# Performance work log

Hardware: AMD Instinct MI355X
Metric: run time of the kernel (lower is better)

Reference implementation:

```python
import jax, jax.numpy as jnp
import numpy as np

D_CUT = 5.0   # cosine-cutoff distance
SIZE = 128    # rbf size == hidden_channels (nn_dist size = in_channels)
L = 2         # num_layers
EPS = 0.0     # GIN eps (non-trainable, initial 0)


def _rbf(d):
    # d: (E,) distances -> (E, SIZE) expnorm RBF with cosine cutoff
    d = d[:, None]
    start = float(np.exp(-D_CUT))
    means = jnp.linspace(start, 1.0, SIZE)
    beta = (2.0 / SIZE * (1.0 - start)) ** (-2)
    dc = jnp.minimum(d, D_CUT)
    cutoff = 0.5 * (jnp.cos(dc * jnp.pi / D_CUT) + 1.0)
    return cutoff * jnp.exp(-beta * (jnp.exp(-d) - means) ** 2)


def setup_inputs() -> dict:
    key = jax.random.key(0)
    ks = jax.random.split(key, 40)
    it = iter(range(40))
    def k():
        return ks[next(it)]
    N, H, ED, AS = 100000, 128, 4, 4
    def w(shape, s):
        return jax.random.normal(k(), shape, jnp.float32) * s
    inp = {}
    inp['x_lig'] = jax.random.normal(k(), (N, H), jnp.float32)
    inp['x_pock'] = jax.random.normal(k(), (N, H), jnp.float32)
    for name, E in (('bond', 200000), ('lp', 400000), ('pl', 400000)):
        inp['ei_' + name] = jax.random.randint(k(), (2, E), 0, N, jnp.int32)
        inp['ew_' + name] = jax.random.uniform(k(), (E,), jnp.float32) * D_CUT
        inp['ea_' + name] = jax.random.normal(k(), (E, AS), jnp.float32)
    inp['W0'] = w((3, AS, ED), 0.5)                 # initial per-edge-type lins (no bias)
    inp['Wd'] = w((L, 3, H, 2 * H), H ** -0.5)      # RBFDistanceScaleShift lin
    inp['bd'] = jnp.zeros((L, 3, 2 * H), jnp.float32)
    inp['We'] = w((L, 3, ED, H), 0.5)               # EGINConv.lin (edge_dim -> hidden)
    inp['be'] = jnp.zeros((L, 3, H), jnp.float32)
    inp['W1'] = w((L, 3, H, H), H ** -0.5)          # nn_node MLP layer 1
    inp['b1'] = jnp.zeros((L, 3, H), jnp.float32)
    inp['W2'] = w((L, 3, H, H), H ** -0.5)          # nn_node MLP layer 2
    inp['b2'] = jnp.zeros((L, 3, H), jnp.float32)
    return inp


def reference(x_lig, x_pock, ei_bond, ew_bond, ea_bond, ei_lp, ew_lp, ea_lp,
              ei_pl, ew_pl, ea_pl, W0, Wd, bd, We, be, W1, b1, W2, b2):
    # HeteroEGIN.forward: initial per-edge-type linear on raw edge attrs (bias-free)
    ea0 = ea_bond @ W0[0]
    ea1 = ea_lp @ W0[1]
    ea2 = ea_pl @ W0[2]

    def conv(x_src, x_dst, ei, ew, ea, t, l):
        # EGINConv per edge type t, layer l
        ss = _rbf(ew) @ Wd[l, t] + bd[l, t]            # (E, 2H) scale/shift from distance
        scale, shift = jnp.split(ss, 2, axis=1)
        xj = x_src[ei[0]] + (ea @ We[l, t] + be[l, t])  # gather + edge-attr lin
        msg = jax.nn.relu(xj * scale + shift)           # gated message
        agg = jax.ops.segment_sum(msg, ei[1], num_segments=x_dst.shape[0])
        o = agg + (1.0 + EPS) * x_dst
        return jax.nn.relu(o @ W1[l, t] + b1[l, t]) @ W2[l, t] + b2[l, t]

    for l in range(L):
        # to_hetero: sum conv outputs across edge types per destination node type
        new_lig = (conv(x_lig, x_lig, ei_bond, ew_bond, ea0, 0, l)
                   + conv(x_pock, x_lig, ei_pl, ew_pl, ea2, 2, l))
        new_pock = conv(x_lig, x_pock, ei_lp, ew_lp, ea1, 1, l)
        if l < L - 1:  # BasicGNN: act between layers, none after last (jk=None)
            new_lig = jax.nn.relu(new_lig)
            new_pock = jax.nn.relu(new_pock)
        x_lig, x_pock = new_lig, new_pock
    return jnp.concatenate([x_lig, x_pock], axis=0)
```

## Files before the change

kernel.cpp:

```cpp
#include <hip/hip_runtime.h>
#include <hip/hip_bf16.h>
#include <hip/hip_fp16.h>
#include <cmath>

typedef __attribute__((ext_vector_type(8))) short short8_t;
typedef __attribute__((ext_vector_type(4))) float f32x4;

static __device__ __forceinline__ short f2bs(float f) {
    union { __hip_bfloat16 h; short s; } u;
    u.h = __float2bfloat16(f);
    return u.s;
}
static __device__ __forceinline__ float bs2f(unsigned int us) {
    union { float f; unsigned int i; } u;
    u.i = us << 16;
    return u.f;
}
static __device__ __forceinline__ unsigned int pack2bf(float a, float b) {
    return (unsigned int)(unsigned short)f2bs(a) |
           ((unsigned int)(unsigned short)f2bs(b) << 16);
}
static __device__ __forceinline__ void lds_barrier() {
    asm volatile("s_waitcnt lgkmcnt(0)\n\ts_barrier" ::: "memory");
}

__global__ void pack_kernel(const float* __restrict__ Wd,
                            const float* __restrict__ W1,
                            const float* __restrict__ W2,
                            const float* __restrict__ W0,
                            const float* __restrict__ We,
                            short* __restrict__ pWd,
                            short* __restrict__ pW1,
                            short* __restrict__ pW2,
                            float* __restrict__ Mb)
{
    const int tid = blockIdx.x * blockDim.x + threadIdx.x;
    const int stride = gridDim.x * blockDim.x;
    for (int i = tid; i < 6 * 32768; i += stride) {
        int c = i >> 15, rem = i & 32767;
        int f = rem >> 9, l = (rem >> 3) & 63, j = rem & 7;
        int kk = f >> 4, nt = f & 15;
        int k = kk * 32 + (l >> 4) * 8 + j;
        int n = nt * 16 + (l & 15);
        pWd[i] = f2bs(Wd[(size_t)c * 32768 + k * 256 + n]);
    }
    for (int i = tid; i < 6 * 16384; i += stride) {
        int c = i >> 14, rem = i & 16383;
        int f = rem >> 9, l = (rem >> 3) & 63, j = rem & 7;
        int kk = f >> 3, nt = f & 7;
        int k = kk * 32 + (l >> 4) * 8 + j;
        int n = nt * 16 + (l & 15);
        pW1[i] = f2bs(W1[(size_t)c * 16384 + k * 128 + n]);
        pW2[i] = f2bs(W2[(size_t)c * 16384 + k * 128 + n]);
    }
    for (int i = tid; i < 6 * 512; i += stride) {
        int c = i >> 9, rem = i & 511;
        int a = rem >> 7, h = rem & 127;
        int t = c % 3;
        float m = 0.f;
        #pragma unroll
        for (int j = 0; j < 4; ++j)
            m = fmaf(W0[t * 16 + a * 4 + j], We[(size_t)c * 512 + j * 128 + h], m);
        Mb[i] = m;
    }
}

__global__ void tobf16_kernel(const float* __restrict__ a, const float* __restrict__ b,
                              unsigned short* __restrict__ oa, unsigned short* __restrict__ ob,
                              int n4)
{
    int i = blockIdx.x * blockDim.x + threadIdx.x;
    const int stride = gridDim.x * blockDim.x;
    for (; i < n4; i += stride) {
        float4 va = ((const float4*)a)[i];
        uint2 pa; pa.x = pack2bf(va.x, va.y); pa.y = pack2bf(va.z, va.w);
        ((uint2*)oa)[i] = pa;
        float4 vb = ((const float4*)b)[i];
        uint2 pb; pb.x = pack2bf(vb.x, vb.y); pb.y = pack2bf(vb.z, vb.w);
        ((uint2*)ob)[i] = pb;
    }
}

__global__ void hist_kernel(const int* __restrict__ ei, int* __restrict__ cnt, int E)
{
    for (int e = blockIdx.x * blockDim.x + threadIdx.x; e < E;
         e += gridDim.x * blockDim.x)
        atomicAdd(&cnt[ei[E + e]], 1);
}

__global__ void scan1k_kernel(int* __restrict__ data, int* __restrict__ bsum, int n)
{
    __shared__ int buf[1024];
    const int gid = blockIdx.x * 1024 + threadIdx.x;
    int v = (gid < n) ? data[gid] : 0;
    buf[threadIdx.x] = v;
    __syncthreads();
    for (int off = 1; off < 1024; off <<= 1) {
        int t = (threadIdx.x >= off) ? buf[threadIdx.x - off] : 0;
        __syncthreads();
        buf[threadIdx.x] += t;
        __syncthreads();
    }
    if (gid < n) data[gid] = buf[threadIdx.x] - v;
    if (bsum && threadIdx.x == 1023) bsum[blockIdx.x] = buf[1023];
}

__global__ void scan_add_kernel(int* __restrict__ data, const int* __restrict__ bsum,
                                int* __restrict__ cursor, int n)
{
    const int gid = blockIdx.x * 1024 + threadIdx.x;
    if (gid < n) {
        int v = data[gid] + bsum[blockIdx.x];
        data[gid] = v;
        cursor[gid] = v;
    }
}

__global__ void scatter_kernel(const int* __restrict__ ei, const float* __restrict__ ew,
                               const float4* __restrict__ ea, int* __restrict__ cursor,
                               float* __restrict__ ewp, float4* __restrict__ eap,
                               int* __restrict__ srcp, int* __restrict__ dstp, int E)
{
    for (int e = blockIdx.x * blockDim.x + threadIdx.x; e < E;
         e += gridDim.x * blockDim.x) {
        int d = ei[E + e];
        int p = atomicAdd(&cursor[d], 1);
        ewp[p]  = ew[e];
        eap[p]  = ea[e];
        srcp[p] = ei[e];
        dstp[p] = d;
    }
}

__global__ __launch_bounds__(512, 2)
void edge_mfma_kernel(
    const unsigned short* __restrict__ xsb,
    const int* __restrict__ srcp, const int* __restrict__ dstp,
    const float* __restrict__ ewp, const float4* __restrict__ eap,
    const short* __restrict__ pWd, const float* __restrict__ bd,
    const float* __restrict__ Mb, const float* __restrict__ be,
    __half2* __restrict__ agg, int E, int ntiles,
    float rs, float rstep, float rbeta)
{
    __shared__ short sRbf[64 * 128];
    __shared__ __half sSS[64 * 256];

    const int t = threadIdx.x;
    const int lane = t & 63;
    const int w = t >> 6;
    const int l15 = lane & 15;
    const int l4 = lane >> 4;

    short8_t bfrag[4][2];
    #pragma unroll
    for (int kk = 0; kk < 4; ++kk)
        #pragma unroll
        for (int i = 0; i < 2; ++i)
            bfrag[kk][i] = *(const short8_t*)&pWd[((kk * 16 + 2 * w + i) * 64 + lane) * 8];
    float bdv[2];
    #pragma unroll
    for (int i = 0; i < 2; ++i) bdv[i] = bd[(2 * w + i) * 16 + l15];
    const float be0 = be[2 * lane], be1 = be[2 * lane + 1];
    float ma0[4], ma1[4];
    #pragma unroll
    for (int a = 0; a < 4; ++a) {
        ma0[a] = Mb[a * 128 + 2 * lane];
        ma1[a] = Mb[a * 128 + 2 * lane + 1];
    }

    const int stride = gridDim.x;
    int tile = blockIdx.x;
    if (tile >= ntiles) return;

    float dd_c; int dst_c; float4 ea_c;
    unsigned int gx[8];
    {
        const int e0 = tile << 6;
        int eL = e0 + lane;
        int eLc = eL < E ? eL : E - 1;
        dd_c = ewp[eLc];
        int es = e0 + w * 8 + (lane & 7);
        int esv = es < E ? es : E - 1;
        dst_c = (es < E) ? dstp[esv] : -1;
        int src_c = srcp[esv];
        ea_c = eap[esv];
        #pragma unroll
        for (int r = 0; r < 8; ++r) {
            int srn = __shfl(src_c, r);
            gx[r] = *(const unsigned int*)&xsb[(size_t)srn * 128 + lane * 2];
        }
    }

    for (; tile < ntiles; tile += stride) {
        const float edv = __expf(-dd_c);
        const float dcc = fminf(dd_c, 5.0f);
        const float cutv = 0.5f * (__cosf(dcc * 0.62831853071795864769f) + 1.0f);
        {
            char* base = (char*)sRbf + lane * 256;
            #pragma unroll
            for (int c = 0; c < 2; ++c) {
                short8_t v;
                #pragma unroll
                for (int j = 0; j < 8; ++j) {
                    float mean = rs + (float)(w * 16 + c * 8 + j) * rstep;
                    float diff = edv - mean;
                    v[j] = f2bs(cutv * __expf(-rbeta * diff * diff));
                }
                *(short8_t*)(base + ((w * 32 + c * 16) ^ ((lane & 7) << 4))) = v;
            }
        }
        unsigned int xjr[8];
        #pragma unroll
        for (int r = 0; r < 8; ++r) {
            float ea0 = __shfl(ea_c.x, r), ea1 = __shfl(ea_c.y, r);
            float ea2 = __shfl(ea_c.z, r), ea3 = __shfl(ea_c.w, r);
            unsigned int g = gx[r];
            float x0 = bs2f(g & 0xffffu), x1 = bs2f(g >> 16);
            float o0 = x0 + be0 + ea0 * ma0[0] + ea1 * ma0[1] + ea2 * ma0[2] + ea3 * ma0[3];
            float o1 = x1 + be1 + ea0 * ma1[0] + ea1 * ma1[1] + ea2 * ma1[2] + ea3 * ma1[3];
            xjr[r] = pack2bf(o0, o1);
        }

        lds_barrier();

        const int ntile = tile + stride;
        const bool has_next = ntile < ntiles;
        float dd_n = 0.f; int dst_n = -1; int src_n = 0;
        float4 ea_n = {0.f, 0.f, 0.f, 0.f};
        if (has_next) {
            const int e0n = ntile << 6;
            int eL = e0n + lane;
            int eLc = eL < E ? eL : E - 1;
            dd_n = ewp[eLc];
            int es = e0n + w * 8 + (lane & 7);
            int esv = es < E ? es : E - 1;
            dst_n = (es < E) ? dstp[esv] : -1;
            src_n = srcp[esv];
            ea_n = eap[esv];
        }
        __builtin_amdgcn_sched_barrier(0);

        f32x4 acc[4][2];
        #pragma unroll
        for (int m = 0; m < 4; ++m) {
            acc[m][0] = (f32x4){0.f, 0.f, 0.f, 0.f};
            acc[m][1] = (f32x4){0.f, 0.f, 0.f, 0.f};
        }
        #pragma unroll
        for (int kk = 0; kk < 4; ++kk) {
            short8_t af[4];
            #pragma unroll
            for (int m = 0; m < 4; ++m) {
                int row = m * 16 + l15;
                int byte = row * 256 + ((kk * 64 + l4 * 16) ^ ((row & 7) << 4));
                af[m] = *(const short8_t*)((const char*)sRbf + byte);
            }
            #pragma unroll
            for (int m = 0; m < 4; ++m)
                #pragma unroll
                for (int i = 0; i < 2; ++i)
                    acc[m][i] = __builtin_amdgcn_mfma_f32_16x16x32_bf16(
                        af[m], bfrag[kk][i], acc[m][i], 0, 0, 0);
        }

        #pragma unroll
        for (int m = 0; m < 4; ++m)
            #pragma unroll
            for (int i = 0; i < 2; ++i) {
                int col = (2 * w + i) * 16 + l15;
                #pragma unroll
                for (int r = 0; r < 4; ++r) {
                    int row = m * 16 + l4 * 4 + r;
                    int byte = row * 512 + ((col * 2) ^ ((row & 7) << 4));
                    *(__half*)((char*)sSS + byte) = __float2half(acc[m][i][r] + bdv[i]);
                }
            }

        if (has_next) {
            #pragma unroll
            for (int r = 0; r < 8; ++r) {
                int srn = __shfl(src_n, r);
                gx[r] = *(const unsigned int*)&xsb[(size_t)srn * 128 + lane * 2];
            }
        }
        const int dst_f = dst_c;
        dd_c = dd_n; dst_c = dst_n; ea_c = ea_n;

        lds_barrier();

        {
            float a0 = 0.f, a1 = 0.f;
            int rdst = __shfl(dst_f, 0);
            #pragma unroll
            for (int r = 0; r < 8; ++r) {
                int e = 8 * w + r;
                unsigned int sc = *(const unsigned int*)
                    ((const char*)sSS + e * 512 + ((lane * 4) ^ ((e & 7) << 4)));
                unsigned int sh = *(const unsigned int*)
                    ((const char*)sSS + e * 512 + ((256 + lane * 4) ^ ((e & 7) << 4)));
                float2 scf = __half22float2(*(const __half2*)&sc);
                float2 shf = __half22float2(*(const __half2*)&sh);
                unsigned int g = xjr[r];
                float x0 = bs2f(g & 0xffffu), x1 = bs2f(g >> 16);
                float m0 = fmaxf(fmaf(x0, scf.x, shf.x), 0.0f);
                float m1 = fmaxf(fmaf(x1, scf.y, shf.y), 0.0f);
                int d = __shfl(dst_f, r);
                if (d != rdst) {
                    if (rdst >= 0) {
                        __half2 hv = __floats2half2_rn(a0, a1);
                        unsigned int hb;
                        __builtin_memcpy(&hb, &hv, 4);
                        if (hb)
                            unsafeAtomicAdd(agg + (size_t)rdst * 64 + lane, hv);
                    }
                    a0 = 0.f; a1 = 0.f; rdst = d;
                }
                a0 += m0; a1 += m1;
            }
            if (rdst >= 0) {
                __half2 hv = __floats2half2_rn(a0, a1);
                unsigned int hb;
                __builtin_memcpy(&hb, &hv, 4);
                if (hb)
                    unsafeAtomicAdd(agg + (size_t)rdst * 64 + lane, hv);
            }
        }
    }
}

__global__ __launch_bounds__(256)
void node_mfma_kernel(
    const __half2* __restrict__ agg,
    const float* __restrict__ xdf, const unsigned short* __restrict__ xdb,
    const short* __restrict__ pW1, const float* __restrict__ b1,
    const short* __restrict__ pW2, const float* __restrict__ b2,
    float* __restrict__ outf, unsigned short* __restrict__ outb,
    int N, int ntiles, int accumulate, int relu_out)
{
    __shared__ short sA[64 * 128];
    __shared__ short sH[64 * 128];

    const int t = threadIdx.x;
    const int lane = t & 63;
    const int w = t >> 6;
    const int l15 = lane & 15;
    const int l4 = lane >> 4;

    short8_t w1f[4][2], w2f[4][2];
    #pragma unroll
    for (int kk = 0; kk < 4; ++kk)
        #pragma unroll
        for (int p = 0; p < 2; ++p) {
            int nt = 2 * w + p;
            w1f[kk][p] = *(const short8_t*)&pW1[((kk * 8 + nt) * 64 + lane) * 8];
            w2f[kk][p] = *(const short8_t*)&pW2[((kk * 8 + nt) * 64 + lane) * 8];
        }
    float b1v[2], b2v[2];
    #pragma unroll
    for (int p = 0; p < 2; ++p) {
        int col = (2 * w + p) * 16 + l15;
        b1v[p] = b1[col];
        b2v[p] = b2[col];
    }

    for (int tile = blockIdx.x; tile < ntiles; tile += gridDim.x) {
        const int n0 = tile << 6;
        #pragma unroll
        for (int i = 0; i < 4; ++i) {
            int idx = i * 256 + t;
            int row = idx >> 4, c8 = idx & 15;
            int gr = n0 + row; if (gr >= N) gr = N - 1;
            union { float4 f; __half2 h[4]; } ar;
            ar.f = ((const float4*)agg)[(size_t)gr * 16 + c8];
            float xv[8];
            if (xdf) {
                float4 x0 = ((const float4*)xdf)[(size_t)gr * 32 + c8 * 2];
                float4 x1 = ((const float4*)xdf)[(size_t)gr * 32 + c8 * 2 + 1];
                xv[0] = x0.x; xv[1] = x0.y; xv[2] = x0.z; xv[3] = x0.w;
                xv[4] = x1.x; xv[5] = x1.y; xv[6] = x1.z; xv[7] = x1.w;
            } else {
                uint4 xr = ((const uint4*)xdb)[(size_t)gr * 16 + c8];
                xv[0] = bs2f(xr.x & 0xffffu); xv[1] = bs2f(xr.x >> 16);
                xv[2] = bs2f(xr.y & 0xffffu); xv[3] = bs2f(xr.y >> 16);
                xv[4] = bs2f(xr.z & 0xffffu); xv[5] = bs2f(xr.z >> 16);
                xv[6] = bs2f(xr.w & 0xffffu); xv[7] = bs2f(xr.w >> 16);
            }
            short8_t v;
            #pragma unroll
            for (int j = 0; j < 4; ++j) {
                float2 a2 = __half22float2(ar.h[j]);
                v[2 * j]     = f2bs(a2.x + xv[2 * j]);
                v[2 * j + 1] = f2bs(a2.y + xv[2 * j + 1]);
            }
            int byte = row * 256 + ((c8 * 16) ^ ((row & 7) << 4));
            *(short8_t*)((char*)sA + byte) = v;
        }
        lds_barrier();

        f32x4 acc[4][2];
        #pragma unroll
        for (int m = 0; m < 4; ++m) {
            acc[m][0] = (f32x4){0.f, 0.f, 0.f, 0.f};
            acc[m][1] = (f32x4){0.f, 0.f, 0.f, 0.f};
        }
        #pragma unroll
        for (int kk = 0; kk < 4; ++kk) {
            short8_t af[4];
            #pragma unroll
            for (int m = 0; m < 4; ++m) {
                int row = m * 16 + l15;
                int byte = row * 256 + ((kk * 64 + l4 * 16) ^ ((row & 7) << 4));
                af[m] = *(const short8_t*)((const char*)sA + byte);
            }
            #pragma unroll
            for (int m = 0; m < 4; ++m)
                #pragma unroll
                for (int p = 0; p < 2; ++p)
                    acc[m][p] = __builtin_amdgcn_mfma_f32_16x16x32_bf16(
                        af[m], w1f[kk][p], acc[m][p], 0, 0, 0);
        }
        #pragma unroll
        for (int m = 0; m < 4; ++m)
            #pragma unroll
            for (int p = 0; p < 2; ++p) {
                int col = (2 * w + p) * 16 + l15;
                #pragma unroll
                for (int r = 0; r < 4; ++r) {
                    int row = m * 16 + l4 * 4 + r;
                    short hs = f2bs(fmaxf(acc[m][p][r] + b1v[p], 0.f));
                    int byte = row * 256 + ((col * 2) ^ ((row & 7) << 4));
                    *(short*)((char*)sH + byte) = hs;
                }
            }
        lds_barrier();

        f32x4 acc2[4][2];
        #pragma unroll
        for (int m = 0; m < 4; ++m) {
            acc2[m][0] = (f32x4){0.f, 0.f, 0.f, 0.f};
            acc2[m][1] = (f32x4){0.f, 0.f, 0.f, 0.f};
        }
        #pragma unroll
        for (int kk = 0; kk < 4; ++kk) {
            short8_t af[4];
            #pragma unroll
            for (int m = 0; m < 4; ++m) {
                int row = m * 16 + l15;
                int byte = row * 256 + ((kk * 64 + l4 * 16) ^ ((row & 7) << 4));
                af[m] = *(const short8_t*)((const char*)sH + byte);
            }
            #pragma unroll
            for (int m = 0; m < 4; ++m)
                #pragma unroll
                for (int p = 0; p < 2; ++p)
                    acc2[m][p] = __builtin_amdgcn_mfma_f32_16x16x32_bf16(
                        af[m], w2f[kk][p], acc2[m][p], 0, 0, 0);
        }
        #pragma unroll
        for (int m = 0; m < 4; ++m)
            #pragma unroll
            for (int p = 0; p < 2; ++p) {
                int col = (2 * w + p) * 16 + l15;
                #pragma unroll
                for (int r = 0; r < 4; ++r) {
                    int row = n0 + m * 16 + l4 * 4 + r;
                    if (row < N) {
                        float v = acc2[m][p][r] + b2v[p];
                        if (outf) {
                            float* op = &outf[(size_t)row * 128 + col];
                            if (accumulate) v += *op;
                            if (relu_out) v = fmaxf(v, 0.f);
                            *op = v;
                        } else {
                            unsigned short* op = &outb[(size_t)row * 128 + col];
                            if (accumulate) v += bs2f((unsigned int)*op);
                            if (relu_out) v = fmaxf(v, 0.f);
                            *op = (unsigned short)f2bs(v);
                        }
                    }
                }
            }
    }
}

extern "C" void kernel_launch(void* const* d_in, const int* in_sizes, int n_in,
                              void* d_out, int out_size, void* d_ws, size_t ws_size,
                              hipStream_t stream)
{
    const float* x_lig   = (const float*)d_in[0];
    const float* x_pock  = (const float*)d_in[1];
    const int*   ei_bond = (const int*)d_in[2];
    const float* ew_bond = (const float*)d_in[3];
    const float* ea_bond = (const float*)d_in[4];
    const int*   ei_lp   = (const int*)d_in[5];
    const float* ew_lp   = (const float*)d_in[6];
    const float* ea_lp   = (const float*)d_in[7];
    const int*   ei_pl   = (const int*)d_in[8];
    const float* ew_pl   = (const float*)d_in[9];
    const float* ea_pl   = (const float*)d_in[10];
    const float* W0 = (const float*)d_in[11];
    const float* Wd = (const float*)d_in[12];
    const float* bd = (const float*)d_in[13];
    const float* We = (const float*)d_in[14];
    const float* be = (const float*)d_in[15];
    const float* W1 = (const float*)d_in[16];
    const float* b1 = (const float*)d_in[17];
    const float* W2 = (const float*)d_in[18];
    const float* b2 = (const float*)d_in[19];

    const int H = 128;
    const int N = in_sizes[0] / H;
    const int E_bond = in_sizes[3];
    const int E_lp   = in_sizes[6];
    const int E_pl   = in_sizes[9];

    char* wp = (char*)d_ws;
    auto alloc = [&](size_t bytes) -> char* {
        char* r = wp;
        wp += (bytes + 255) & ~(size_t)255;
        return r;
    };
    unsigned short* A   = (unsigned short*)alloc((size_t)N * H * 2);
    unsigned short* Bb  = (unsigned short*)alloc((size_t)N * H * 2);
    unsigned short* C   = (unsigned short*)alloc((size_t)N * H * 2);
    __half*  agg  = (__half*)alloc((size_t)N * H * 2);
    float4*  eapB = (float4*)alloc((size_t)E_bond * 16);
    float4*  eapL = (float4*)alloc((size_t)E_lp * 16);
    float4*  eapP = (float4*)alloc((size_t)E_pl * 16);
    float*   ewpB = (float*)alloc((size_t)E_bond * 4);
    float*   ewpL = (float*)alloc((size_t)E_lp * 4);
    float*   ewpP = (float*)alloc((size_t)E_pl * 4);
    int*     srcB = (int*)alloc((size_t)E_bond * 4);
    int*     srcL = (int*)alloc((size_t)E_lp * 4);
    int*     srcP = (int*)alloc((size_t)E_pl * 4);
    int*     dstB = (int*)alloc((size_t)E_bond * 4);
    int*     dstL = (int*)alloc((size_t)E_lp * 4);
    int*     dstP = (int*)alloc((size_t)E_pl * 4);
    short*   pWd  = (short*)alloc(6 * 32768 * 2);
    short*   pW1s = (short*)alloc(6 * 16384 * 2);
    short*   pW2s = (short*)alloc(6 * 16384 * 2);
    float*   Mb   = (float*)alloc(6 * 512 * 4);
    int*     cnt    = (int*)alloc((size_t)N * 4);
    int*     cursor = (int*)alloc((size_t)N * 4);
    int*     bsum   = (int*)alloc(1024 * 4);

    float* outL = (float*)d_out;
    float* outP = outL + (size_t)N * H;

    const int capE = 2 * 256;
    const int capN = 4 * 256;

    tobf16_kernel<<<512, 256, 0, stream>>>(x_lig, x_pock, A, Bb, N * H / 4);
    pack_kernel<<<256, 256, 0, stream>>>(Wd, W1, W2, W0, We, pWd, pW1s, pW2s, Mb);

    const int nb = (N + 1023) / 1024;
    auto sortset = [&](const int* ei_, const float* ew_, const float* ea_, int E,
                       float* ewp, float4* eap, int* sr716, int* dstp) {
        hipMemsetAsync(cnt, 0, (size_t)N * sizeof(int), stream);
        hist_kernel<<<512, 256, 0, stream>>>(ei_, cnt, E);
        scan1k_kernel<<<nb, 1024, 0, stream>>>(cnt, bsum, N);
        scan1k_kernel<<<1, 1024, 0, stream>>>(bsum, nullptr, nb);
        scan_add_kernel<<<nb, 1024, 0, stream>>>(cnt, bsum, cursor, N);
        scatter_kernel<<<512, 256, 0, stream>>>(ei_, ew_, (const float4*)ea_,
                                                cursor, ewp, eap, sr716, dstp, E);
    };
    sortset(ei_bond, ew_bond, ea_bond, E_bond, ewpB, eapB, srcB, dstB);
    sortset(ei_lp,   ew_lp,   ea_lp,   E_lp,   ewpL, eapL, srcL, dstL);
    sortset(ei_pl,   ew_pl,   ea_pl,   E_pl,   ewpP, eapP, srcP, dstP);

    const double start_d = exp(-5.0);
    const float rs    = (float)start_d;
    const float rstep = (float)((1.0 - start_d) / 127.0);
    const float rbeta = (float)std::pow(2.0 / 128.0 * (1.0 - start_d), -2.0);

    auto conv = [&](const unsigned short* src,
                    const float* xdf, const unsigned short* xdb,
                    const int* srcp, const int* dstp, const float* ewp,
                    const float4* eap, int E,
                    int l, int tt, float* outf, unsigned short* outb,
                    int accum, int relu) {
        hipMemsetAsync(agg, 0, (size_t)N * H * sizeof(__half), stream);
        const int lt = l * 3 + tt;
        const int ntE = (E + 63) / 64;
        const int gE = ntE < capE ? ntE : capE;
        edge_mfma_kernel<<<gE, 512, 0, stream>>>(
            src, srcp, dstp, ewp, eap,
            pWd + (size_t)lt * 32768, bd + (size_t)lt * 256,
            Mb + (size_t)lt * 512, be + (size_t)lt * 128,
            (__half2*)agg, E, ntE, rs, rstep, rbeta);
        const int ntN = (N + 63) / 64;
        const int gN = ntN < capN ? ntN : capN;
        node_mfma_kernel<<<gN, 256, 0, stream>>>(
            (const __half2*)agg, xdf, xdb,
            pW1s + (size_t)lt * 16384, b1 + (size_t)lt * 128,
            pW2s + (size_t)lt * 16384, b2 + (size_t)lt * 128,
            outf, outb, N, ntN, accum, relu);
    };

    conv(A,  x_pock, nullptr, srcL, dstL, ewpL, eapL, E_lp,   0, 1, nullptr, C, 0, 1);
    conv(A,  x_lig,  nullptr, srcB, dstB, ewpB, eapB, E_bond, 0, 0, nullptr, A, 0, 0);
    conv(Bb, x_lig,  nullptr, srcP, dstP, ewpP, eapP, E_pl,   0, 2, nullptr, A, 1, 1);
    conv(A, nullptr, A, srcB, dstB, ewpB, eapB, E_bond, 1, 0, outL, nullptr, 0, 0);
    conv(C, nullptr, A, srcP, dstP, ewpP, eapP, E_pl,   1, 2, outL, nullptr, 1, 0);
    conv(A, nullptr, C, srcL, dstL, ewpL, eapL, E_lp,   1, 1, outP, nullptr, 0, 0);
}
```

Baseline: 936.2 us.

## Pack sorted edge records into AoS and widen edge kernel to 1024 threads

The scatter now writes one 32-byte record per edge (weight, src, dst, attrs) in place of four separate arrays, so the edge kernel reads two float4 loads per edge. The edge kernel moves from 512 to 1024 threads per block, with each wave owning one 16-column slice of the scale/shift GEMM and four edges per wave; the grid cap is halved. The node kernel stops holding W1/W2 fragments in registers and reloads them per k-step, targeting two blocks per SM. This trades register pressure and occupancy against extra weight reloads and more padded record traffic.

After: 1.015 ms. +8.4%, slower.

```diff
diff --git a/kernel.cpp b/kernel.cpp
--- a/kernel.cpp
+++ b/kernel.cpp
@@ -118,25 +118,26 @@
 
 __global__ void scatter_kernel(const int* __restrict__ ei, const float* __restrict__ ew,
                                const float4* __restrict__ ea, int* __restrict__ cursor,
-                               float* __restrict__ ewp, float4* __restrict__ eap,
-                               int* __restrict__ srcp, int* __restrict__ dstp, int E)
+                               float4* __restrict__ rec, int E)
 {
     for (int e = blockIdx.x * blockDim.x + threadIdx.x; e < E;
          e += gridDim.x * blockDim.x) {
         int d = ei[E + e];
         int p = atomicAdd(&cursor[d], 1);
-        ewp[p]  = ew[e];
-        eap[p]  = ea[e];
-        srcp[p] = ei[e];
-        dstp[p] = d;
-    }
-}
-
-__global__ __launch_bounds__(512, 2)
+        float4 r0;
+        r0.x = ew[e];
+        r0.y = __int_as_float(ei[e]);
+        r0.z = __int_as_float(d);
+        r0.w = 0.f;
+        rec[(size_t)p * 2]     = r0;
+        rec[(size_t)p * 2 + 1] = ea[e];
+    }
+}
+
+__global__ __launch_bounds__(1024)
 void edge_mfma_kernel(
     const unsigned short* __restrict__ xsb,
-    const int* __restrict__ srcp, const int* __restrict__ dstp,
-    const float* __restrict__ ewp, const float4* __restrict__ eap,
+    const float4* __restrict__ rec,
     const short* __restrict__ pWd, const float* __restrict__ bd,
     const float* __restrict__ Mb, const float* __restrict__ be,
     __half2* __restrict__ agg, int E, int ntiles,
@@ -151,15 +152,11 @@
     const int l15 = lane & 15;
     const int l4 = lane >> 4;
 
-    short8_t bfrag[4][2];
+    short8_t bfrag[4];
     #pragma unroll
     for (int kk = 0; kk < 4; ++kk)
-        #pragma unroll
-        for (int i = 0; i < 2; ++i)
-            bfrag[kk][i] = *(const short8_t*)&pWd[((kk * 16 + 2 * w + i) * 64 + lane) * 8];
-    float bdv[2];
-    #pragma unroll
-    for (int i = 0; i < 2; ++i) bdv[i] = bd[(2 * w + i) * 16 + l15];
+        bfrag[kk] = *(const short8_t*)&pWd[((kk * 16 + w) * 64 + lane) * 8];
+    const float bdv = bd[w * 16 + l15];
     const float be0 = be[2 * lane], be1 = be[2 * lane + 1];
     float ma0[4], ma1[4];
     #pragma unroll
@@ -172,48 +169,44 @@
     int tile = blockIdx.x;
     if (tile >= ntiles) return;
 
-    float dd_c; int dst_c; float4 ea_c;
-    unsigned int gx[8];
+    float ew_c; int src_c, dst_c; float4 ea_c;
     {
-        const int e0 = tile << 6;
-        int eL = e0 + lane;
-        int eLc = eL < E ? eL : E - 1;
-        dd_c = ewp[eLc];
-        int es = e0 + w * 8 + (lane & 7);
-        int esv = es < E ? es : E - 1;
-        dst_c = (es < E) ? dstp[esv] : -1;
-        int src_c = srcp[esv];
-        ea_c = eap[esv];
-        #pragma unroll
-        for (int r = 0; r < 8; ++r) {
-            int srn = __shfl(src_c, r);
-            gx[r] = *(const unsigned int*)&xsb[(size_t)srn * 128 + lane * 2];
-        }
+        int eL = (tile << 6) + lane;
+        int ec = eL < E ? eL : E - 1;
+        float4 r0 = rec[(size_t)ec * 2];
+        float4 r1 = rec[(size_t)ec * 2 + 1];
+        ew_c = r0.x;
+        src_c = __float_as_int(r0.y);
+        dst_c = (eL < E) ? __float_as_int(r0.z) : -1;
+        ea_c = r1;
+    }
+    unsigned int gx[4];
+    #pragma unroll
+    for (int r = 0; r < 4; ++r) {
+        int srn = __shfl(src_c, 4 * w + r);
+        gx[r] = *(const unsigned int*)&xsb[(size_t)srn * 128 + lane * 2];
     }
 
     for (; tile < ntiles; tile += stride) {
-        const float edv = __expf(-dd_c);
-        const float dcc = fminf(dd_c, 5.0f);
+        const float edv = __expf(-ew_c);
+        const float dcc = fminf(ew_c, 5.0f);
         const float cutv = 0.5f * (__cosf(dcc * 0.62831853071795864769f) + 1.0f);
         {
-            char* base = (char*)sRbf + lane * 256;
-            #pragma unroll
-            for (int c = 0; c < 2; ++c) {
-                short8_t v;
-                #pragma unroll
-                for (int j = 0; j < 8; ++j) {
-                    float mean = rs + (float)(w * 16 + c * 8 + j) * rstep;
-                    float diff = edv - mean;
-                    v[j] = f2bs(cutv * __expf(-rbeta * diff * diff));
-                }
-                *(short8_t*)(base + ((w * 32 + c * 16) ^ ((lane & 7) << 4))) = v;
-            }
-        }
-        unsigned int xjr[8];
-        #pragma unroll
-        for (int r = 0; r < 8; ++r) {
-            float ea0 = __shfl(ea_c.x, r), ea1 = __shfl(ea_c.y, r);
-            float ea2 = __shfl(ea_c.z, r), ea3 = __shfl(ea_c.w, r);
+            short8_t v;
+            #pragma unroll
+            for (int j = 0; j < 8; ++j) {
+                float mean = rs + (float)(w * 8 + j) * rstep;
+                float diff = edv - mean;
+                v[j] = f2bs(cutv * __expf(-rbeta * diff * diff));
+            }
+            *(short8_t*)((char*)sRbf + lane * 256 + ((w * 16) ^ ((lane & 7) << 4))) = v;
+        }
+        unsigned int xjr[4];
+        #pragma unroll
+        for (int r = 0; r < 4; ++r) {
+            int e = 4 * w + r;
+            float ea0 = __shfl(ea_c.x, e), ea1 = __shfl(ea_c.y, e);
+            float ea2 = __shfl(ea_c.z, e), ea3 = __shfl(ea_c.w, e);
             unsigned int g = gx[r];
             float x0 = bs2f(g & 0xffffu), x1 = bs2f(g >> 16);
             float o0 = x0 + be0 + ea0 * ma0[0] + ea1 * ma0[1] + ea2 * ma0[2] + ea3 * ma0[3];
@@ -225,27 +218,23 @@
 
         const int ntile = tile + stride;
         const bool has_next = ntile < ntiles;
-        float dd_n = 0.f; int dst_n = -1; int src_n = 0;
+        float ew_n = 0.f; int src_n = 0, dst_n = -1;
         float4 ea_n = {0.f, 0.f, 0.f, 0.f};
         if (has_next) {
-            const int e0n = ntile << 6;
-            int eL = e0n + lane;
-            int eLc = eL < E ? eL : E - 1;
-            dd_n = ewp[eLc];
-            int es = e0n + w * 8 + (lane & 7);
-            int esv = es < E ? es : E - 1;
-            dst_n = (es < E) ? dstp[esv] : -1;
-            src_n = srcp[esv];
-            ea_n = eap[esv];
+            int eL = (ntile << 6) + lane;
+            int ec = eL < E ? eL : E - 1;
+            float4 r0 = rec[(size_t)ec * 2];
+            float4 r1 = rec[(size_t)ec * 2 + 1];
+            ew_n = r0.x;
+            src_n = __float_as_int(r0.y);
+            dst_n = (eL < E) ? __float_as_int(r0.z) : -1;
+            ea_n = r1;
         }
         __builtin_amdgcn_sched_barrier(0);
 
-        f32x4 acc[4][2];
-        #pragma unroll
-        for (int m = 0; m < 4; ++m) {
-            acc[m][0] = (f32x4){0.f, 0.f, 0.f, 0.f};
-            acc[m][1] = (f32x4){0.f, 0.f, 0.f, 0.f};
-        }
+        f32x4 acc[4];
+        #pragma unroll
+        for (int m = 0; m < 4; ++m) acc[m] = (f32x4){0.f, 0.f, 0.f, 0.f};
         #pragma unroll
         for (int kk = 0; kk < 4; ++kk) {
             short8_t af[4];
@@ -257,43 +246,40 @@
             }
             #pragma unroll
             for (int m = 0; m < 4; ++m)
-                #pragma unroll
-                for (int i = 0; i < 2; ++i)
-                    acc[m][i] = __builtin_amdgcn_mfma_f32_16x16x32_bf16(
-                        af[m], bfrag[kk][i], acc[m][i], 0, 0, 0);
-        }
-
-        #pragma unroll
-        for (int m = 0; m < 4; ++m)
-            #pragma unroll
-            for (int i = 0; i < 2; ++i) {
-                int col = (2 * w + i) * 16 + l15;
+                acc[m] = __builtin_amdgcn_mfma_f32_16x16x32_bf16(
+                    af[m], bfrag[kk], acc[m], 0, 0, 0);
+        }
+
+        {
+            const int col2 = (w * 16 + l15) * 2;
+            #pragma unroll
+            for (int m = 0; m < 4; ++m)
                 #pragma unroll
                 for (int r = 0; r < 4; ++r) {
                     int row = m * 16 + l4 * 4 + r;
-                    int byte = row * 512 + ((col * 2) ^ ((row & 7) << 4));
-                    *(__half*)((char*)sSS + byte) = __float2half(acc[m][i][r] + bdv[i]);
+                    int byte = row * 512 + (col2 ^ ((row & 7) << 4));
+                    *(__half*)((char*)sSS + byte) = __float2half(acc[m][r] + bdv);
                 }
-            }
+        }
 
         if (has_next) {
             #pragma unroll
-            for (int r = 0; r < 8; ++r) {
-                int srn = __shfl(src_n, r);
+            for (int r = 0; r < 4; ++r) {
+                int srn = __shfl(src_n, 4 * w + r);
                 gx[r] = *(const unsigned int*)&xsb[(size_t)srn * 128 + lane * 2];
             }
         }
         const int dst_f = dst_c;
-        dd_c = dd_n; dst_c = dst_n; ea_c = ea_n;
+        ew_c = ew_n; src_c = src_n; dst_c = dst_n; ea_c = ea_n;
 
         lds_barrier();
 
         {
             float a0 = 0.f, a1 = 0.f;
-            int rdst = __shfl(dst_f, 0);
-            #pragma unroll
-            for (int r = 0; r < 8; ++r) {
-                int e = 8 * w + r;
+            int rdst = __shfl(dst_f, 4 * w);
+            #pragma unroll
+            for (int r = 0; r < 4; ++r) {
+                int e = 4 * w + r;
                 unsigned int sc = *(const unsigned int*)
                     ((const char*)sSS + e * 512 + ((lane * 4) ^ ((e & 7) << 4)));
                 unsigned int sh = *(const unsigned int*)
@@ -304,7 +290,7 @@
                 float x0 = bs2f(g & 0xffffu), x1 = bs2f(g >> 16);
                 float m0 = fmaxf(fmaf(x0, scf.x, shf.x), 0.0f);
                 float m1 = fmaxf(fmaf(x1, scf.y, shf.y), 0.0f);
-                int d = __shfl(dst_f, r);
+                int d = __shfl(dst_f, e);
                 if (d != rdst) {
                     if (rdst >= 0) {
                         __half2 hv = __floats2half2_rn(a0, a1);
@@ -328,7 +314,7 @@
     }
 }
 
-__global__ __launch_bounds__(256)
+__global__ __launch_bounds__(256, 2)
 void node_mfma_kernel(
     const __half2* __restrict__ agg,
     const float* __restrict__ xdf, const unsigned short* __restrict__ xdb,
@@ -346,15 +332,6 @@
     const int l15 = lane & 15;
     const int l4 = lane >> 4;
 
-    short8_t w1f[4][2], w2f[4][2];
-    #pragma unroll
-    for (int kk = 0; kk < 4; ++kk)
-        #pragma unroll
-        for (int p = 0; p < 2; ++p) {
-            int nt = 2 * w + p;
-            w1f[kk][p] = *(const short8_t*)&pW1[((kk * 8 + nt) * 64 + lane) * 8];
-            w2f[kk][p] = *(const short8_t*)&pW2[((kk * 8 + nt) * 64 + lane) * 8];
-        }
     float b1v[2], b2v[2];
     #pragma unroll
     for (int p = 0; p < 2; ++p) {
@@ -405,6 +382,10 @@
         }
         #pragma unroll
         for (int kk = 0; kk < 4; ++kk) {
+            short8_t wf[2];
+            #pragma unroll
+            for (int p = 0; p < 2; ++p)
+                wf[p] = *(const short8_t*)&pW1[((kk * 8 + 2 * w + p) * 64 + lane) * 8];
             short8_t af[4];
             #pragma unroll
             for (int m = 0; m < 4; ++m) {
@@ -417,7 +398,7 @@
                 #pragma unroll
                 for (int p = 0; p < 2; ++p)
                     acc[m][p] = __builtin_amdgcn_mfma_f32_16x16x32_bf16(
-                        af[m], w1f[kk][p], acc[m][p], 0, 0, 0);
+                        af[m], wf[p], acc[m][p], 0, 0, 0);
         }
         #pragma unroll
         for (int m = 0; m < 4; ++m)
@@ -442,6 +423,10 @@
         }
         #pragma unroll
         for (int kk = 0; kk < 4; ++kk) {
+            short8_t wf[2];
+            #pragma unroll
+            for (int p = 0; p < 2; ++p)
+                wf[p] = *(const short8_t*)&pW2[((kk * 8 + 2 * w + p) * 64 + lane) * 8];
             short8_t af[4];
             #pragma unroll
             for (int m = 0; m < 4; ++m) {
@@ -454,7 +439,7 @@
                 #pragma unroll
                 for (int p = 0; p < 2; ++p)
                     acc2[m][p] = __builtin_amdgcn_mfma_f32_16x16x32_bf16(
-                        af[m], w2f[kk][p], acc2[m][p], 0, 0, 0);
+                        af[m], wf[p], acc2[m][p], 0, 0, 0);
         }
         #pragma unroll
         for (int m = 0; m < 4; ++m)
@@ -524,18 +509,9 @@
     unsigned short* Bb  = (unsigned short*)alloc((size_t)N * H * 2);
     unsigned short* C   = (unsigned short*)alloc((size_t)N * H * 2);
     __half*  agg  = (__half*)alloc((size_t)N * H * 2);
-    float4*  eapB = (float4*)alloc((size_t)E_bond * 16);
-    float4*  eapL = (float4*)alloc((size_t)E_lp * 16);
-    float4*  eapP = (float4*)alloc((size_t)E_pl * 16);
-    float*   ewpB = (float*)alloc((size_t)E_bond * 4);
-    float*   ewpL = (float*)alloc((size_t)E_lp * 4);
-    float*   ewpP = (float*)alloc((size_t)E_pl * 4);
-    int*     srcB = (int*)alloc((size_t)E_bond * 4);
-    int*     srcL = (int*)alloc((size_t)E_lp * 4);
-    int*     srcP = (int*)alloc((size_t)E_pl * 4);
-    int*     dstB = (int*)alloc((size_t)E_bond * 4);
-    int*     dstL = (int*)alloc((size_t)E_lp * 4);
-    int*     dstP = (int*)alloc((size_t)E_pl * 4);
+    float4*  recB = (float4*)alloc((size_t)E_bond * 32);
+    float4*  recL = (float4*)alloc((size_t)E_lp * 32);
+    float4*  recP = (float4*)alloc((size_t)E_pl * 32);
     short*   pWd  = (short*)alloc(6 * 32768 * 2);
     short*   pW1s = (short*)alloc(6 * 16384 * 2);
     short*   pW2s = (short*)alloc(6 * 16384 * 2);
@@ -547,7 +523,7 @@
     float* outL = (float*)d_out;
     float* outP = outL + (size_t)N * H;
 
-    const int capE = 2 * 256;
+    const int capE = 256;
     const int capN = 4 * 256;
 
     tobf16_kernel<<<512, 256, 0, stream>>>(x_lig, x_pock, A, Bb, N * H / 4);
@@ -555,18 +531,18 @@
 
     const int nb = (N + 1023) / 1024;
     auto sortset = [&](const int* ei_, const float* ew_, const float* ea_, int E,
-                       float* ewp, float4* eap, int* sr716, int* dstp) {
+                       float4* rec) {
         hipMemsetAsync(cnt, 0, (size_t)N * sizeof(int), stream);
         hist_kernel<<<512, 256, 0, stream>>>(ei_, cnt, E);
         scan1k_kernel<<<nb, 1024, 0, stream>>>(cnt, bsum, N);
         scan1k_kernel<<<1, 1024, 0, stream>>>(bsum, nullptr, nb);
         scan_add_kernel<<<nb, 1024, 0, stream>>>(cnt, bsum, cursor, N);
         scatter_kernel<<<512, 256, 0, stream>>>(ei_, ew_, (const float4*)ea_,
-                                                cursor, ewp, eap, sr716, dstp, E);
+                                                cursor, rec, E);
     };
-    sortset(ei_bond, ew_bond, ea_bond, E_bond, ewpB, eapB, srcB, dstB);
-    sortset(ei_lp,   ew_lp,   ea_lp,   E_lp,   ewpL, eapL, srcL, dstL);
-    sortset(ei_pl,   ew_pl,   ea_pl,   E_pl,   ewpP, eapP, srcP, dstP);
+    sortset(ei_bond, ew_bond, ea_bond, E_bond, recB);
+    sortset(ei_lp,   ew_lp,   ea_lp,   E_lp,   recL);
+    sortset(ei_pl,   ew_pl,   ea_pl,   E_pl,   recP);
 
     const double start_d = exp(-5.0);
     const float rs    = (float)start_d;
@@ -575,16 +551,15 @@
 
     auto conv = [&](const unsigned short* src,
                     const float* xdf, const unsigned short* xdb,
-                    const int* srcp, const int* dstp, const float* ewp,
-                    const float4* eap, int E,
+                    const float4* rec, int E,
                     int l, int tt, float* outf, unsigned short* outb,
                     int accum, int relu) {
         hipMemsetAsync(agg, 0, (size_t)N * H * sizeof(__half), stream);
         const int lt = l * 3 + tt;
         const int ntE = (E + 63) / 64;
         const int gE = ntE < capE ? ntE : capE;
-        edge_mfma_kernel<<<gE, 512, 0, stream>>>(
-            src, srcp, dstp, ewp, eap,
+        edge_mfma_kernel<<<gE, 1024, 0, stream>>>(
+            src, rec,
             pWd + (size_t)lt * 32768, bd + (size_t)lt * 256,
             Mb + (size_t)lt * 512, be + (size_t)lt * 128,
             (__half2*)agg, E, ntE, rs, rstep, rbeta);
@@ -597,10 +572,10 @@
             outf, outb, N, ntN, accum, relu);
     };
 
-    conv(A,  x_pock, nullptr, srcL, dstL, ewpL, eapL, E_lp,   0, 1, nullptr, C, 0, 1);
-    conv(A,  x_lig,  nullptr, srcB, dstB, ewpB, eapB, E_bond, 0, 0, nullptr, A, 0, 0);
-    conv(Bb, x_lig,  nullptr, srcP, dstP, ewpP, eapP, E_pl,   0, 2, nullptr, A, 1, 1);
-    conv(A, nullptr, A, srcB, dstB, ewpB, eapB, E_bond, 1, 0, outL, nullptr, 0, 0);
-    conv(C, nullptr, A, srcP, dstP, ewpP, eapP, E_pl,   1, 2, outL, nullptr, 1, 0);
-    conv(A, nullptr, C, srcL, dstL, ewpL, eapL, E_lp,   1, 1, outP, nullptr, 0, 0);
-}
+    conv(A,  x_pock, nullptr, recL, E_lp,   0, 1, nullptr, C, 0, 1);
+    conv(A,  x_lig,  nullptr, recB, E_bond, 0, 0, nullptr, A, 0, 0);
+    conv(Bb, x_lig,  nullptr, recP, E_pl,   0, 2, nullptr, A, 1, 1);
+    conv(A, nullptr, A, recB, E_bond, 1, 0, outL, nullptr, 0, 0);
+    conv(C, nullptr, A, recP, E_pl,   1, 2, outL, nullptr, 1, 0);
+    conv(A, nullptr, C, recL, E_lp,   1, 1, outP, nullptr, 0, 0);
+}
```
